# Performance work log

Measured on AMD Instinct MI355X. Metric: run time of the kernel, lower is better.

Reference implementation:

```python
import jax, jax.numpy as jnp
import numpy as np

N, Tq, Tk = 4096, 48, 48
E, H = 64, 4
HD = E // H
TN = 288            # time_num (5-min slots per day)
FE = 4              # forward_expansion
EPS = 1e-5


def _ln(x, g, b):
    mu = jnp.mean(x, axis=-1, keepdims=True)
    var = jnp.var(x, axis=-1, keepdims=True)
    return (x - mu) * jax.lax.rsqrt(var + EPS) * g + b


def setup_inputs() -> dict:
    rng = jax.random.key(0)
    ks = jax.random.split(rng, 12)
    s = 0.05
    return {
        "value": jax.random.normal(ks[0], (N, Tk, E), jnp.float32),
        "keys": jax.random.normal(ks[1], (N, Tk, E), jnp.float32),
        "query": jax.random.normal(ks[2], (N, Tq, E), jnp.float32),
        "Wv": jax.random.normal(ks[3], (HD, HD), jnp.float32) * s,
        "Wk": jax.random.normal(ks[4], (HD, HD), jnp.float32) * s,
        "Wq": jax.random.normal(ks[5], (HD, HD), jnp.float32) * s,
        "Wo": jax.random.normal(ks[6], (E, E), jnp.float32) * s,
        "bo": jnp.zeros((E,), jnp.float32),
        "temb": jax.random.normal(ks[7], (TN, E), jnp.float32) * s,
        "ln1_g": jnp.ones((E,), jnp.float32),
        "ln1_b": jnp.zeros((E,), jnp.float32),
        "ln2_g": jnp.ones((E,), jnp.float32),
        "ln2_b": jnp.zeros((E,), jnp.float32),
        "W1": jax.random.normal(ks[8], (FE * E, E), jnp.float32) * s,  # torch Linear(E, FE*E).weight
        "b1": jnp.zeros((FE * E,), jnp.float32),
        "W2": jax.random.normal(ks[9], (E, FE * E), jnp.float32) * s,
        "b2": jnp.zeros((E,), jnp.float32),
        "tq": 10,
    }


def reference(value, keys, query, Wv, Wk, Wq, Wo, bo, temb,
              ln1_g, ln1_b, ln2_g, ln2_b, W1, b1, W2, b2, tq):
    # temporal embedding add (tk = tq since tk=-1 default)
    tq_inds = (TN + tq + jnp.arange(Tq)) % TN
    tk_inds = (TN + tq + jnp.arange(Tk)) % TN
    q = query + temb[tq_inds][None, :, :]   # (N,Tq,E)
    k = keys + temb[tk_inds][None, :, :]    # (N,Tk,E)

    qh = q.reshape(N, Tq, H, HD)
    kh = k.reshape(N, Tk, H, HD)
    vh = value.reshape(N, Tk, H, HD)
    # per-head small linear projections (x @ W.T, no bias)
    qh = jnp.einsum('nthd,ed->nthe', qh, Wq)
    kh = jnp.einsum('nthd,ed->nthe', kh, Wk)
    vh = jnp.einsum('nthd,ed->nthe', vh, Wv)

    energy = jnp.einsum('nqhd,nkhd->nqkh', qh, kh)  # (N,Tq,Tk,H)
    # causal mask (mask=True path): masked entries set to -1e6 BEFORE scale+clamp
    tmask = jnp.tril(jnp.ones((Tq, Tk), jnp.float32))
    energy = jnp.where(tmask[None, :, :, None] == 0, jnp.float32(-1e6), energy)
    logits = jnp.clip(energy / jnp.float32(np.sqrt(E)), -5.0, 5.0)
    attention = jax.nn.softmax(logits, axis=2)       # softmax over k

    out = jnp.einsum('nqkh,nkhd->nqhd', attention, vh).reshape(N, Tq, E)
    out = out @ Wo.T + bo

    x = _ln(out + q, ln1_g, ln1_b)                   # dropout is identity (eval)
    ff = jax.nn.relu(x @ W1.T + b1) @ W2.T + b2
    return _ln(ff + x, ln2_g, ln2_b)
```

## Files before the change

kernel.cpp:

```cpp
#include <hip/hip_runtime.h>
#include <hip/hip_bf16.h>
#include <math.h>

#define NSEQ 4096
#define TN 288
#define EPSF 1e-5f

typedef short bf16x8 __attribute__((ext_vector_type(8)));
typedef float f32x4 __attribute__((ext_vector_type(4)));

#define WSV 0
#define WSK 256
#define WSQ 512
#define WSO 768
#define WS1 4864
#define WS2 21248

#define A_S   0
#define B_S   3456
#define C_S   6912
#define D_S   10496
#define CD_F  3456
#define H_S   6912

__device__ __forceinline__ unsigned short f2bf_u(float f) {
    __hip_bfloat16 h = __float2bfloat16(f);
    return *reinterpret_cast<const unsigned short*>(&h);
}
__device__ __forceinline__ unsigned int pk2(float a, float b) {
    return (unsigned int)f2bf_u(a) | ((unsigned int)f2bf_u(b) << 16);
}
__device__ __forceinline__ float bits2f(unsigned int u) { return __uint_as_float(u); }

__global__ void wconv_kernel(const float* __restrict__ Wv, const float* __restrict__ Wk,
                             const float* __restrict__ Wq, const float* __restrict__ Wo,
                             const float* __restrict__ W1, const float* __restrict__ W2,
                             short* __restrict__ ws) {
    int i = blockIdx.x * 256 + threadIdx.x;
    float v;
    if (i < 256)        v = Wv[i];
    else if (i < 512)   v = Wk[i - 256];
    else if (i < 768)   v = Wq[i - 512] * 0.125f;
    else if (i < 4864)  v = Wo[i - 768];
    else if (i < 21248) v = W1[i - 4864];
    else                v = W2[i - 21248];
    ws[i] = (short)f2bf_u(v);
}

__global__ __launch_bounds__(256, 5)
void ttrans_kernel(const float* __restrict__ value,
                   const float* __restrict__ keys,
                   const float* __restrict__ query,
                   const float* __restrict__ bo,
                   const float* __restrict__ temb,
                   const float* __restrict__ ln1g,
                   const float* __restrict__ ln1b,
                   const float* __restrict__ ln2g,
                   const float* __restrict__ ln2b,
                   const float* __restrict__ pb1,
                   const float* __restrict__ pb2,
                   const short* __restrict__ ws,
                   const int* __restrict__ tqp,
                   float* __restrict__ out)
{
    __shared__ __align__(16) unsigned char smem[27136];
    short* S16 = reinterpret_cast<short*>(smem);
    float* S32 = reinterpret_cast<float*>(smem);

    const int tid  = threadIdx.x;
    const int lane = tid & 63;
    const int w    = tid >> 6;
    const int l15  = lane & 15;
    const int lg   = lane >> 4;
    const int n    = blockIdx.x;
    const size_t gbase = (size_t)n * 3072;
    const int tqv  = *tqp;
    const int c4   = (lane & 15) * 4;
    const int rg   = lane >> 4;
    const int hh   = w;

    float4 qres4[3];
    {
        int t = w * 12 + rg;
        int ti = ((tqv % TN) + TN + t) % TN;
        #pragma unroll
        for (int it = 0; it < 3; ++it) {
            float4 tv = *reinterpret_cast<const float4*>(&temb[ti * 64 + c4]);
            float4 qv = *reinterpret_cast<const float4*>(&query[gbase + t * 64 + c4]);
            float4 kv = *reinterpret_cast<const float4*>(&keys [gbase + t * 64 + c4]);
            float4 vv = *reinterpret_cast<const float4*>(&value[gbase + t * 64 + c4]);
            float4 qq = make_float4(qv.x + tv.x, qv.y + tv.y, qv.z + tv.z, qv.w + tv.w);
            float4 kk = make_float4(kv.x + tv.x, kv.y + tv.y, kv.z + tv.z, kv.w + tv.w);
            qres4[it] = qq;
            *reinterpret_cast<uint2*>(&S16[A_S + t * 72 + c4]) =
                make_uint2(pk2(qq.x, qq.y), pk2(qq.z, qq.w));
            *reinterpret_cast<uint2*>(&S16[B_S + t * 72 + c4]) =
                make_uint2(pk2(kk.x, kk.y), pk2(kk.z, kk.w));
            *reinterpret_cast<uint2*>(&S16[C_S + t * 72 + c4]) =
                make_uint2(pk2(vv.x, vv.y), pk2(vv.z, vv.w));
            t += 4; ti += 4; if (ti >= TN) ti -= TN;
        }
    }
    __syncthreads();

    {
        bf16x8 bWv = {}, bWk = {}, bWq = {};
        if (lane < 32) {
            bWv = *reinterpret_cast<const bf16x8*>(&ws[WSV + l15 * 16 + lg * 8]);
            bWk = *reinterpret_cast<const bf16x8*>(&ws[WSK + l15 * 16 + lg * 8]);
            bWq = *reinterpret_cast<const bf16x8*>(&ws[WSQ + l15 * 16 + lg * 8]);
        }
        #pragma unroll
        for (int rt = 0; rt < 3; ++rt) {
            bf16x8 aQ = {}, aK = {}, aV = {};
            if (lane < 32) {
                int ro = (rt * 16 + l15) * 72 + hh * 16 + lg * 8;
                aQ = *reinterpret_cast<const bf16x8*>(&S16[A_S + ro]);
                aK = *reinterpret_cast<const bf16x8*>(&S16[B_S + ro]);
                aV = *reinterpret_cast<const bf16x8*>(&S16[C_S + ro]);
            }
            f32x4 z = {0.f,0.f,0.f,0.f};
            f32x4 cQ = __builtin_amdgcn_mfma_f32_16x16x32_bf16(aQ, bWq, z, 0, 0, 0);
            f32x4 cK = __builtin_amdgcn_mfma_f32_16x16x32_bf16(aK, bWk, z, 0, 0, 0);
            f32x4 cV = __builtin_amdgcn_mfma_f32_16x16x32_bf16(aV, bWv, z, 0, 0, 0);
            #pragma unroll
            for (int r = 0; r < 4; ++r) {
                int row = rt * 16 + lg * 4 + r;
                S16[A_S + row * 72 + hh * 16 + l15] = (short)f2bf_u(cQ[r]);
                S16[B_S + row * 72 + hh * 16 + l15] = (short)f2bf_u(cK[r]);
                S16[D_S + (hh * 16 + l15) * 48 + row] = (short)f2bf_u(cV[r]);
            }
        }
    }
    __syncthreads();

    {
        const float PEXP = 0.006737946999085467f;
        const unsigned short PBF = f2bf_u(PEXP);
        bf16x8 bK0 = {}, bK1 = {}, bK2 = {};
        if (lane < 32) {
            bK0 = *reinterpret_cast<const bf16x8*>(&S16[B_S + ( 0 + l15) * 72 + hh * 16 + lg * 8]);
            bK1 = *reinterpret_cast<const bf16x8*>(&S16[B_S + (16 + l15) * 72 + hh * 16 + lg * 8]);
            bK2 = *reinterpret_cast<const bf16x8*>(&S16[B_S + (32 + l15) * 72 + hh * 16 + lg * 8]);
        }
        bf16x8 vA = *reinterpret_cast<const bf16x8*>(&S16[D_S + (hh * 16 + l15) * 48 + lg * 8]);
        bf16x8 vB = {};
        if (lane < 32)
            vB = *reinterpret_cast<const bf16x8*>(&S16[D_S + (hh * 16 + l15) * 48 + 32 + lg * 8]);

        #pragma unroll
        for (int rt = 0; rt < 3; ++rt) {
            bf16x8 aQ = {};
            if (lane < 32)
                aQ = *reinterpret_cast<const bf16x8*>(&S16[A_S + (rt * 16 + l15) * 72 + hh * 16 + lg * 8]);
            f32x4 z = {0.f,0.f,0.f,0.f};
            f32x4 e0 = __builtin_amdgcn_mfma_f32_16x16x32_bf16(aQ, bK0, z, 0, 0, 0);
            f32x4 e1 = z, e2 = z;
            if (rt >= 1) e1 = __builtin_amdgcn_mfma_f32_16x16x32_bf16(aQ, bK1, z, 0, 0, 0);
            if (rt == 2) e2 = __builtin_amdgcn_mfma_f32_16x16x32_bf16(aQ, bK2, z, 0, 0, 0);
            const int abase = C_S + hh * 896;
            float inv[4];
            #pragma unroll
            for (int r = 0; r < 4; ++r) {
                int tl = lg * 4 + r;
                int t = rt * 16 + tl;
                float p0, p1, p2;
                float v0 = fminf(5.f, fmaxf(-5.f, e0[r]));
                if (rt == 0) v0 = (l15 <= t) ? v0 : -5.f;
                p0 = __expf(v0);
                S16[abase + tl * 56 + l15] = (short)f2bf_u(p0);
                if (rt == 0) {
                    p1 = PEXP;
                    S16[abase + tl * 56 + 16 + l15] = (short)PBF;
                } else {
                    float v1 = fminf(5.f, fmaxf(-5.f, e1[r]));
                    if (rt == 1) v1 = (16 + l15 <= t) ? v1 : -5.f;
                    p1 = __expf(v1);
                    S16[abase + tl * 56 + 16 + l15] = (short)f2bf_u(p1);
                }
                if (rt < 2) {
                    p2 = PEXP;
                    S16[abase + tl * 56 + 32 + l15] = (short)PBF;
                } else {
                    float v2c = fminf(5.f, fmaxf(-5.f, e2[r]));
                    v2c = (32 + l15 <= t) ? v2c : -5.f;
                    p2 = __expf(v2c);
                    S16[abase + tl * 56 + 32 + l15] = (short)f2bf_u(p2);
                }
                float s = p0 + p1 + p2;
                s += __shfl_xor(s, 1);
                s += __shfl_xor(s, 2);
                s += __shfl_xor(s, 4);
                s += __shfl_xor(s, 8);
                inv[r] = __builtin_amdgcn_rcpf(s);
            }
            bf16x8 a0 = *reinterpret_cast<const bf16x8*>(&S16[abase + l15 * 56 + lg * 8]);
            bf16x8 a1 = {};
            if (lane < 32)
                a1 = *reinterpret_cast<const bf16x8*>(&S16[abase + l15 * 56 + 32 + lg * 8]);
            f32x4 zz = {0.f,0.f,0.f,0.f};
            f32x4 oc = __builtin_amdgcn_mfma_f32_16x16x32_bf16(a0, vA, zz, 0, 0, 0);
            oc = __builtin_amdgcn_mfma_f32_16x16x32_bf16(a1, vB, oc, 0, 0, 0);
            #pragma unroll
            for (int r = 0; r < 4; ++r)
                S16[B_S + (rt * 16 + lg * 4 + r) * 72 + hh * 16 + l15] =
                    (short)f2bf_u(oc[r] * inv[r]);
        }
    }
    __syncthreads();

    {
        bf16x8 bO0 = *reinterpret_cast<const bf16x8*>(&ws[WSO + (w * 16 + l15) * 64 + lg * 8]);
        bf16x8 bO1 = *reinterpret_cast<const bf16x8*>(&ws[WSO + (w * 16 + l15) * 64 + 32 + lg * 8]);
        const float bo_v = bo[w * 16 + l15];
        #pragma unroll
        for (int mt = 0; mt < 3; ++mt) {
            bf16x8 a0 = *reinterpret_cast<const bf16x8*>(&S16[B_S + (mt * 16 + l15) * 72 + lg * 8]);
            bf16x8 a1 = *reinterpret_cast<const bf16x8*>(&S16[B_S + (mt * 16 + l15) * 72 + 32 + lg * 8]);
            f32x4 c = {0.f,0.f,0.f,0.f};
            c = __builtin_amdgcn_mfma_f32_16x16x32_bf16(a0, bO0, c, 0, 0, 0);
            c = __builtin_amdgcn_mfma_f32_16x16x32_bf16(a1, bO1, c, 0, 0, 0);
            #pragma unroll
            for (int r = 0; r < 4; ++r)
                S32[CD_F + (mt * 16 + lg * 4 + r) * 68 + w * 16 + l15] = c[r] + bo_v;
        }
    }
    __syncthreads();

    {
        float4 g1 = *reinterpret_cast<const float4*>(&ln1g[c4]);
        float4 be1 = *reinterpret_cast<const float4*>(&ln1b[c4]);
        #pragma unroll
        for (int it = 0; it < 3; ++it) {
            int t = w * 12 + it * 4 + rg;
            float4 o = *reinterpret_cast<const float4*>(&S32[CD_F + t * 68 + c4]);
            float v0 = o.x + qres4[it].x, v1 = o.y + qres4[it].y;
            float v2 = o.z + qres4[it].z, v3 = o.w + qres4[it].w;
            float s1 = (v0 + v1) + (v2 + v3);
            float s2 = (v0 * v0 + v1 * v1) + (v2 * v2 + v3 * v3);
            s1 += __shfl_xor(s1, 1); s1 += __shfl_xor(s1, 2);
            s1 += __shfl_xor(s1, 4); s1 += __shfl_xor(s1, 8);
            s2 += __shfl_xor(s2, 1); s2 += __shfl_xor(s2, 2);
            s2 += __shfl_xor(s2, 4); s2 += __shfl_xor(s2, 8);
            float mu  = s1 * (1.f / 64.f);
            float var = s2 * (1.f / 64.f) - mu * mu;
            float rs = __builtin_amdgcn_rsqf(var + EPSF);
            float x0 = (v0 - mu) * rs * g1.x + be1.x;
            float x1 = (v1 - mu) * rs * g1.y + be1.y;
            float x2 = (v2 - mu) * rs * g1.z + be1.z;
            float x3 = (v3 - mu) * rs * g1.w + be1.w;
            *reinterpret_cast<uint2*>(&S16[A_S + t * 72 + c4]) =
                make_uint2(pk2(x0, x1), pk2(x2, x3));
        }
    }
    __syncthreads();

    f32x4 ffC[3];
    #pragma unroll
    for (int mt = 0; mt < 3; ++mt) ffC[mt] = (f32x4){0.f,0.f,0.f,0.f};

    #pragma unroll
    for (int hb = 0; hb < 2; ++hb) {
        #pragma unroll
        for (int jj = 0; jj < 2; ++jj) {
            int j16 = w * 2 + jj;
            int jrow = (hb * 8 + j16) * 16 + l15;
            bf16x8 b0 = *reinterpret_cast<const bf16x8*>(&ws[WS1 + jrow * 64 + lg * 8]);
            bf16x8 b1 = *reinterpret_cast<const bf16x8*>(&ws[WS1 + jrow * 64 + 32 + lg * 8]);
            float b1v = pb1[jrow];
            #pragma unroll
            for (int mt = 0; mt < 3; ++mt) {
                bf16x8 a0 = *reinterpret_cast<const bf16x8*>(&S16[A_S + (mt * 16 + l15) * 72 + lg * 8]);
                bf16x8 a1 = *reinterpret_cast<const bf16x8*>(&S16[A_S + (mt * 16 + l15) * 72 + 32 + lg * 8]);
                f32x4 c = {0.f,0.f,0.f,0.f};
                c = __builtin_amdgcn_mfma_f32_16x16x32_bf16(a0, b0, c, 0, 0, 0);
                c = __builtin_amdgcn_mfma_f32_16x16x32_bf16(a1, b1, c, 0, 0, 0);
                #pragma unroll
                for (int r = 0; r < 4; ++r)
                    S16[H_S + (mt * 16 + lg * 4 + r) * 136 + j16 * 16 + l15] =
                        (short)f2bf_u(fmaxf(c[r] + b1v, 0.f));
            }
        }
        __syncthreads();

        {
            const int wb = WS2 + (w * 16 + l15) * 256 + hb * 128;
            bf16x8 bw0 = *reinterpret_cast<const bf16x8*>(&ws[wb +  0 + lg * 8]);
            bf16x8 bw1 = *reinterpret_cast<const bf16x8*>(&ws[wb + 32 + lg * 8]);
            bf16x8 bw2 = *reinterpret_cast<const bf16x8*>(&ws[wb + 64 + lg * 8]);
            bf16x8 bw3 = *reinterpret_cast<const bf16x8*>(&ws[wb + 96 + lg * 8]);
            #pragma unroll
            for (int mt = 0; mt < 3; ++mt) {
                bf16x8 a0 = *reinterpret_cast<const bf16x8*>(&S16[H_S + (mt * 16 + l15) * 136 +  0 + lg * 8]);
                bf16x8 a1 = *reinterpret_cast<const bf16x8*>(&S16[H_S + (mt * 16 + l15) * 136 + 32 + lg * 8]);
                bf16x8 a2 = *reinterpret_cast<const bf16x8*>(&S16[H_S + (mt * 16 + l15) * 136 + 64 + lg * 8]);
                bf16x8 a3 = *reinterpret_cast<const bf16x8*>(&S16[H_S + (mt * 16 + l15) * 136 + 96 + lg * 8]);
                ffC[mt] = __builtin_amdgcn_mfma_f32_16x16x32_bf16(a0, bw0, ffC[mt], 0, 0, 0);
                ffC[mt] = __builtin_amdgcn_mfma_f32_16x16x32_bf16(a1, bw1, ffC[mt], 0, 0, 0);
                ffC[mt] = __builtin_amdgcn_mfma_f32_16x16x32_bf16(a2, bw2, ffC[mt], 0, 0, 0);
                ffC[mt] = __builtin_amdgcn_mfma_f32_16x16x32_bf16(a3, bw3, ffC[mt], 0, 0, 0);
            }
        }
        if (hb == 0) __syncthreads();
    }

    {
        float b2v = pb2[w * 16 + l15];
        #pragma unroll
        for (int mt = 0; mt < 3; ++mt)
            #pragma unroll
            for (int r = 0; r < 4; ++r)
                S16[B_S + (mt * 16 + lg * 4 + r) * 72 + w * 16 + l15] =
                    (short)f2bf_u(ffC[mt][r] + b2v);
    }
    __syncthreads();

    {
        float4 g2 = *reinterpret_cast<const float4*>(&ln2g[c4]);
        float4 be2 = *reinterpret_cast<const float4*>(&ln2b[c4]);
        #pragma unroll
        for (int it = 0; it < 3; ++it) {
            int t = w * 12 + it * 4 + rg;
            uint2 fp = *reinterpret_cast<const uint2*>(&S16[B_S + t * 72 + c4]);
            uint2 xp = *reinterpret_cast<const uint2*>(&S16[A_S + t * 72 + c4]);
            float v0 = bits2f(fp.x << 16) + bits2f(xp.x << 16);
            float v1 = bits2f(fp.x & 0xffff0000u) + bits2f(xp.x & 0xffff0000u);
            float v2 = bits2f(fp.y << 16) + bits2f(xp.y << 16);
            float v3 = bits2f(fp.y & 0xffff0000u) + bits2f(xp.y & 0xffff0000u);
            float s1 = (v0 + v1) + (v2 + v3);
            float s2 = (v0 * v0 + v1 * v1) + (v2 * v2 + v3 * v3);
            s1 += __shfl_xor(s1, 1); s1 += __shfl_xor(s1, 2);
            s1 += __shfl_xor(s1, 4); s1 += __shfl_xor(s1, 8);
            s2 += __shfl_xor(s2, 1); s2 += __shfl_xor(s2, 2);
            s2 += __shfl_xor(s2, 4); s2 += __shfl_xor(s2, 8);
            float mu  = s1 * (1.f / 64.f);
            float var = s2 * (1.f / 64.f) - mu * mu;
            float rs = __builtin_amdgcn_rsqf(var + EPSF);
            float y0 = (v0 - mu) * rs * g2.x + be2.x;
            float y1 = (v1 - mu) * rs * g2.y + be2.y;
            float y2 = (v2 - mu) * rs * g2.z + be2.z;
            float y3 = (v3 - mu) * rs * g2.w + be2.w;
            *reinterpret_cast<float4*>(&out[gbase + t * 64 + c4]) =
                make_float4(y0, y1, y2, y3);
        }
    }
}

extern "C" void kernel_launch(void* const* d_in, const int* in_sizes, int n_in,
                              void* d_out, int out_size, void* d_ws, size_t ws_size,
                              hipStream_t stream) {
    const float* value = (const float*)d_in[0];
    const float* keys  = (const float*)d_in[1];
    const float* query = (const float*)d_in[2];
    const float* Wv    = (const float*)d_in[3];
    const float* Wk    = (const float*)d_in[4];
    const float* Wq    = (const float*)d_in[5];
    const float* Wo    = (const float*)d_in[6];
    const float* bo    = (const float*)d_in[7];
    const float* temb  = (const float*)d_in[8];
    const float* ln1g  = (const float*)d_in[9];
    const float* ln1b  = (const float*)d_in[10];
    const float* ln2g  = (const float*)d_in[11];
    const float* ln2b  = (const float*)d_in[12];
    const float* W1    = (const float*)d_in[13];
    const float* b1    = (const float*)d_in[14];
    const float* W2    = (const float*)d_in[15];
    const float* b2    = (const float*)d_in[16];
    const int*   tq    = (const int*)d_in[17];
    float* outp = (float*)d_out;
    short* ws = (short*)d_ws;

    hipLaunchKernelGGL(wconv_kernel, dim3(147), dim3(256), 0, stream,
                       Wv, Wk, Wq, Wo, W1, W2, ws);
    hipLaunchKernelGGL(ttrans_kernel, dim3(NSEQ), dim3(256), 0, stream,
                       value, keys, query, bo, temb,
                       ln1g, ln1b, ln2g, ln2b, b1, b2, ws, tq, outp);
}
```

Baseline: 74.99 us.

## Make each warp own a row tile through Wo, LN1, FFN and LN2

After attention, the output projection, first layernorm, both FFN matmuls and the final layernorm are restructured so each of three waves owns a 16-row tile and covers all 64 output columns. This drops the block-wide barriers between these stages and the fp32 smem staging buffer, and keeps the LN1 output in registers for the second residual. The Q projection result is also kept in registers and written to a compact per-head smem area so the A buffer can hold the raw q residual. The cost is that the fourth wave sits idle for the whole tail, each wave does four times the FFN MFMA work serially, and the final stores become scalar strided writes instead of float4.

```diff
diff --git a/kernel.cpp b/kernel.cpp
--- a/kernel.cpp
+++ b/kernel.cpp
@@ -20,7 +20,6 @@
 #define B_S   3456
 #define C_S   6912
 #define D_S   10496
-#define CD_F  3456
 #define H_S   6912
 
 __device__ __forceinline__ unsigned short f2bf_u(float f) {
@@ -65,7 +64,6 @@
 {
     __shared__ __align__(16) unsigned char smem[27136];
     short* S16 = reinterpret_cast<short*>(smem);
-    float* S32 = reinterpret_cast<float*>(smem);
 
     const int tid  = threadIdx.x;
     const int lane = tid & 63;
@@ -79,7 +77,6 @@
     const int rg   = lane >> 4;
     const int hh   = w;
 
-    float4 qres4[3];
     {
         int t = w * 12 + rg;
         int ti = ((tqv % TN) + TN + t) % TN;
@@ -91,7 +88,6 @@
             float4 vv = *reinterpret_cast<const float4*>(&value[gbase + t * 64 + c4]);
             float4 qq = make_float4(qv.x + tv.x, qv.y + tv.y, qv.z + tv.z, qv.w + tv.w);
             float4 kk = make_float4(kv.x + tv.x, kv.y + tv.y, kv.z + tv.z, kv.w + tv.w);
-            qres4[it] = qq;
             *reinterpret_cast<uint2*>(&S16[A_S + t * 72 + c4]) =
                 make_uint2(pk2(qq.x, qq.y), pk2(qq.z, qq.w));
             *reinterpret_cast<uint2*>(&S16[B_S + t * 72 + c4]) =
@@ -103,6 +99,7 @@
     }
     __syncthreads();
 
+    f32x4 cQ[3];
     {
         bf16x8 bWv = {}, bWk = {}, bWq = {};
         if (lane < 32) {
@@ -120,13 +117,12 @@
                 aV = *reinterpret_cast<const bf16x8*>(&S16[C_S + ro]);
             }
             f32x4 z = {0.f,0.f,0.f,0.f};
-            f32x4 cQ = __builtin_amdgcn_mfma_f32_16x16x32_bf16(aQ, bWq, z, 0, 0, 0);
+            cQ[rt] = __builtin_amdgcn_mfma_f32_16x16x32_bf16(aQ, bWq, z, 0, 0, 0);
             f32x4 cK = __builtin_amdgcn_mfma_f32_16x16x32_bf16(aK, bWk, z, 0, 0, 0);
             f32x4 cV = __builtin_amdgcn_mfma_f32_16x16x32_bf16(aV, bWv, z, 0, 0, 0);
             #pragma unroll
             for (int r = 0; r < 4; ++r) {
                 int row = rt * 16 + lg * 4 + r;
-                S16[A_S + row * 72 + hh * 16 + l15] = (short)f2bf_u(cQ[r]);
                 S16[B_S + row * 72 + hh * 16 + l15] = (short)f2bf_u(cK[r]);
                 S16[D_S + (hh * 16 + l15) * 48 + row] = (short)f2bf_u(cV[r]);
             }
@@ -137,6 +133,12 @@
     {
         const float PEXP = 0.006737946999085467f;
         const unsigned short PBF = f2bf_u(PEXP);
+        #pragma unroll
+        for (int rt = 0; rt < 3; ++rt)
+            #pragma unroll
+            for (int r = 0; r < 4; ++r)
+                S16[C_S + hh * 768 + (rt * 16 + lg * 4 + r) * 16 + l15] =
+                    (short)f2bf_u(cQ[rt][r]);
         bf16x8 bK0 = {}, bK1 = {}, bK2 = {};
         if (lane < 32) {
             bK0 = *reinterpret_cast<const bf16x8*>(&S16[B_S + ( 0 + l15) * 72 + hh * 16 + lg * 8]);
@@ -152,13 +154,13 @@
         for (int rt = 0; rt < 3; ++rt) {
             bf16x8 aQ = {};
             if (lane < 32)
-                aQ = *reinterpret_cast<const bf16x8*>(&S16[A_S + (rt * 16 + l15) * 72 + hh * 16 + lg * 8]);
+                aQ = *reinterpret_cast<const bf16x8*>(&S16[C_S + hh * 768 + (rt * 16 + l15) * 16 + lg * 8]);
             f32x4 z = {0.f,0.f,0.f,0.f};
             f32x4 e0 = __builtin_amdgcn_mfma_f32_16x16x32_bf16(aQ, bK0, z, 0, 0, 0);
             f32x4 e1 = z, e2 = z;
             if (rt >= 1) e1 = __builtin_amdgcn_mfma_f32_16x16x32_bf16(aQ, bK1, z, 0, 0, 0);
             if (rt == 2) e2 = __builtin_amdgcn_mfma_f32_16x16x32_bf16(aQ, bK2, z, 0, 0, 0);
-            const int abase = C_S + hh * 896;
+            const int abase = D_S + hh * 768;
             float inv[4];
             #pragma unroll
             for (int r = 0; r < 4; ++r) {
@@ -168,24 +170,24 @@
                 float v0 = fminf(5.f, fmaxf(-5.f, e0[r]));
                 if (rt == 0) v0 = (l15 <= t) ? v0 : -5.f;
                 p0 = __expf(v0);
-                S16[abase + tl * 56 + l15] = (short)f2bf_u(p0);
+                S16[abase + tl * 48 + l15] = (short)f2bf_u(p0);
                 if (rt == 0) {
                     p1 = PEXP;
-                    S16[abase + tl * 56 + 16 + l15] = (short)PBF;
+                    S16[abase + tl * 48 + 16 + l15] = (short)PBF;
                 } else {
                     float v1 = fminf(5.f, fmaxf(-5.f, e1[r]));
                     if (rt == 1) v1 = (16 + l15 <= t) ? v1 : -5.f;
                     p1 = __expf(v1);
-                    S16[abase + tl * 56 + 16 + l15] = (short)f2bf_u(p1);
+                    S16[abase + tl * 48 + 16 + l15] = (short)f2bf_u(p1);
                 }
                 if (rt < 2) {
                     p2 = PEXP;
-                    S16[abase + tl * 56 + 32 + l15] = (short)PBF;
+                    S16[abase + tl * 48 + 32 + l15] = (short)PBF;
                 } else {
                     float v2c = fminf(5.f, fmaxf(-5.f, e2[r]));
                     v2c = (32 + l15 <= t) ? v2c : -5.f;
                     p2 = __expf(v2c);
-                    S16[abase + tl * 56 + 32 + l15] = (short)f2bf_u(p2);
+                    S16[abase + tl * 48 + 32 + l15] = (short)f2bf_u(p2);
                 }
                 float s = p0 + p1 + p2;
                 s += __shfl_xor(s, 1);
@@ -194,10 +196,10 @@
                 s += __shfl_xor(s, 8);
                 inv[r] = __builtin_amdgcn_rcpf(s);
             }
-            bf16x8 a0 = *reinterpret_cast<const bf16x8*>(&S16[abase + l15 * 56 + lg * 8]);
+            bf16x8 a0 = *reinterpret_cast<const bf16x8*>(&S16[abase + l15 * 48 + lg * 8]);
             bf16x8 a1 = {};
             if (lane < 32)
-                a1 = *reinterpret_cast<const bf16x8*>(&S16[abase + l15 * 56 + 32 + lg * 8]);
+                a1 = *reinterpret_cast<const bf16x8*>(&S16[abase + l15 * 48 + 32 + lg * 8]);
             f32x4 zz = {0.f,0.f,0.f,0.f};
             f32x4 oc = __builtin_amdgcn_mfma_f32_16x16x32_bf16(a0, vA, zz, 0, 0, 0);
             oc = __builtin_amdgcn_mfma_f32_16x16x32_bf16(a1, vB, oc, 0, 0, 0);
@@ -209,35 +211,37 @@
     }
     __syncthreads();
 
-    {
-        bf16x8 bO0 = *reinterpret_cast<const bf16x8*>(&ws[WSO + (w * 16 + l15) * 64 + lg * 8]);
-        bf16x8 bO1 = *reinterpret_cast<const bf16x8*>(&ws[WSO + (w * 16 + l15) * 64 + 32 + lg * 8]);
-        const float bo_v = bo[w * 16 + l15];
-        #pragma unroll
-        for (int mt = 0; mt < 3; ++mt) {
-            bf16x8 a0 = *reinterpret_cast<const bf16x8*>(&S16[B_S + (mt * 16 + l15) * 72 + lg * 8]);
-            bf16x8 a1 = *reinterpret_cast<const bf16x8*>(&S16[B_S + (mt * 16 + l15) * 72 + 32 + lg * 8]);
-            f32x4 c = {0.f,0.f,0.f,0.f};
-            c = __builtin_amdgcn_mfma_f32_16x16x32_bf16(a0, bO0, c, 0, 0, 0);
-            c = __builtin_amdgcn_mfma_f32_16x16x32_bf16(a1, bO1, c, 0, 0, 0);
-            #pragma unroll
-            for (int r = 0; r < 4; ++r)
-                S32[CD_F + (mt * 16 + lg * 4 + r) * 68 + w * 16 + l15] = c[r] + bo_v;
-        }
-    }
-    __syncthreads();
-
-    {
-        float4 g1 = *reinterpret_cast<const float4*>(&ln1g[c4]);
-        float4 be1 = *reinterpret_cast<const float4*>(&ln1b[c4]);
-        #pragma unroll
-        for (int it = 0; it < 3; ++it) {
-            int t = w * 12 + it * 4 + rg;
-            float4 o = *reinterpret_cast<const float4*>(&S32[CD_F + t * 68 + c4]);
-            float v0 = o.x + qres4[it].x, v1 = o.y + qres4[it].y;
-            float v2 = o.z + qres4[it].z, v3 = o.w + qres4[it].w;
-            float s1 = (v0 + v1) + (v2 + v3);
-            float s2 = (v0 * v0 + v1 * v1) + (v2 * v2 + v3 * v3);
+    if (w < 3) {
+        bf16x8 ao0 = *reinterpret_cast<const bf16x8*>(&S16[B_S + (w * 16 + l15) * 72 + lg * 8]);
+        bf16x8 ao1 = *reinterpret_cast<const bf16x8*>(&S16[B_S + (w * 16 + l15) * 72 + 32 + lg * 8]);
+        f32x4 c[4];
+        #pragma unroll
+        for (int nt = 0; nt < 4; ++nt) {
+            bf16x8 bO0 = *reinterpret_cast<const bf16x8*>(&ws[WSO + (nt * 16 + l15) * 64 + lg * 8]);
+            bf16x8 bO1 = *reinterpret_cast<const bf16x8*>(&ws[WSO + (nt * 16 + l15) * 64 + 32 + lg * 8]);
+            f32x4 z = {0.f,0.f,0.f,0.f};
+            c[nt] = __builtin_amdgcn_mfma_f32_16x16x32_bf16(ao0, bO0, z, 0, 0, 0);
+            c[nt] = __builtin_amdgcn_mfma_f32_16x16x32_bf16(ao1, bO1, c[nt], 0, 0, 0);
+        }
+        float bo4[4], g1v[4], be1v[4];
+        #pragma unroll
+        for (int nt = 0; nt < 4; ++nt) {
+            bo4[nt]  = bo[nt * 16 + l15];
+            g1v[nt]  = ln1g[nt * 16 + l15];
+            be1v[nt] = ln1b[nt * 16 + l15];
+        }
+        float xres[4][4];
+        #pragma unroll
+        for (int r = 0; r < 4; ++r) {
+            int row = w * 16 + lg * 4 + r;
+            float v[4];
+            #pragma unroll
+            for (int nt = 0; nt < 4; ++nt) {
+                unsigned int qb = (unsigned int)(unsigned short)S16[A_S + row * 72 + nt * 16 + l15];
+                v[nt] = c[nt][r] + bo4[nt] + bits2f(qb << 16);
+            }
+            float s1 = (v[0] + v[1]) + (v[2] + v[3]);
+            float s2 = (v[0]*v[0] + v[1]*v[1]) + (v[2]*v[2] + v[3]*v[3]);
             s1 += __shfl_xor(s1, 1); s1 += __shfl_xor(s1, 2);
             s1 += __shfl_xor(s1, 4); s1 += __shfl_xor(s1, 8);
             s2 += __shfl_xor(s2, 1); s2 += __shfl_xor(s2, 2);
@@ -245,90 +249,67 @@
             float mu  = s1 * (1.f / 64.f);
             float var = s2 * (1.f / 64.f) - mu * mu;
             float rs = __builtin_amdgcn_rsqf(var + EPSF);
-            float x0 = (v0 - mu) * rs * g1.x + be1.x;
-            float x1 = (v1 - mu) * rs * g1.y + be1.y;
-            float x2 = (v2 - mu) * rs * g1.z + be1.z;
-            float x3 = (v3 - mu) * rs * g1.w + be1.w;
-            *reinterpret_cast<uint2*>(&S16[A_S + t * 72 + c4]) =
-                make_uint2(pk2(x0, x1), pk2(x2, x3));
-        }
-    }
-    __syncthreads();
-
-    f32x4 ffC[3];
-    #pragma unroll
-    for (int mt = 0; mt < 3; ++mt) ffC[mt] = (f32x4){0.f,0.f,0.f,0.f};
-
-    #pragma unroll
-    for (int hb = 0; hb < 2; ++hb) {
-        #pragma unroll
-        for (int jj = 0; jj < 2; ++jj) {
-            int j16 = w * 2 + jj;
-            int jrow = (hb * 8 + j16) * 16 + l15;
-            bf16x8 b0 = *reinterpret_cast<const bf16x8*>(&ws[WS1 + jrow * 64 + lg * 8]);
-            bf16x8 b1 = *reinterpret_cast<const bf16x8*>(&ws[WS1 + jrow * 64 + 32 + lg * 8]);
-            float b1v = pb1[jrow];
-            #pragma unroll
-            for (int mt = 0; mt < 3; ++mt) {
-                bf16x8 a0 = *reinterpret_cast<const bf16x8*>(&S16[A_S + (mt * 16 + l15) * 72 + lg * 8]);
-                bf16x8 a1 = *reinterpret_cast<const bf16x8*>(&S16[A_S + (mt * 16 + l15) * 72 + 32 + lg * 8]);
-                f32x4 c = {0.f,0.f,0.f,0.f};
-                c = __builtin_amdgcn_mfma_f32_16x16x32_bf16(a0, b0, c, 0, 0, 0);
-                c = __builtin_amdgcn_mfma_f32_16x16x32_bf16(a1, b1, c, 0, 0, 0);
+            #pragma unroll
+            for (int nt = 0; nt < 4; ++nt) {
+                float x = (v[nt] - mu) * rs * g1v[nt] + be1v[nt];
+                xres[r][nt] = x;
+                S16[A_S + row * 72 + nt * 16 + l15] = (short)f2bf_u(x);
+            }
+        }
+        f32x4 ffC[4];
+        #pragma unroll
+        for (int nt = 0; nt < 4; ++nt) ffC[nt] = (f32x4){0.f,0.f,0.f,0.f};
+        bf16x8 aX0 = *reinterpret_cast<const bf16x8*>(&S16[A_S + (w * 16 + l15) * 72 + lg * 8]);
+        bf16x8 aX1 = *reinterpret_cast<const bf16x8*>(&S16[A_S + (w * 16 + l15) * 72 + 32 + lg * 8]);
+        #pragma unroll
+        for (int hb = 0; hb < 2; ++hb) {
+            #pragma unroll
+            for (int j16 = 0; j16 < 8; ++j16) {
+                int jrow = (hb * 8 + j16) * 16 + l15;
+                bf16x8 b0 = *reinterpret_cast<const bf16x8*>(&ws[WS1 + jrow * 64 + lg * 8]);
+                bf16x8 b1 = *reinterpret_cast<const bf16x8*>(&ws[WS1 + jrow * 64 + 32 + lg * 8]);
+                float b1v = pb1[jrow];
+                f32x4 z = {0.f,0.f,0.f,0.f};
+                f32x4 ch = __builtin_amdgcn_mfma_f32_16x16x32_bf16(aX0, b0, z, 0, 0, 0);
+                ch = __builtin_amdgcn_mfma_f32_16x16x32_bf16(aX1, b1, ch, 0, 0, 0);
                 #pragma unroll
                 for (int r = 0; r < 4; ++r)
-                    S16[H_S + (mt * 16 + lg * 4 + r) * 136 + j16 * 16 + l15] =
-                        (short)f2bf_u(fmaxf(c[r] + b1v, 0.f));
-            }
-        }
-        __syncthreads();
-
-        {
-            const int wb = WS2 + (w * 16 + l15) * 256 + hb * 128;
-            bf16x8 bw0 = *reinterpret_cast<const bf16x8*>(&ws[wb +  0 + lg * 8]);
-            bf16x8 bw1 = *reinterpret_cast<const bf16x8*>(&ws[wb + 32 + lg * 8]);
-            bf16x8 bw2 = *reinterpret_cast<const bf16x8*>(&ws[wb + 64 + lg * 8]);
-            bf16x8 bw3 = *reinterpret_cast<const bf16x8*>(&ws[wb + 96 + lg * 8]);
-            #pragma unroll
-            for (int mt = 0; mt < 3; ++mt) {
-                bf16x8 a0 = *reinterpret_cast<const bf16x8*>(&S16[H_S + (mt * 16 + l15) * 136 +  0 + lg * 8]);
-                bf16x8 a1 = *reinterpret_cast<const bf16x8*>(&S16[H_S + (mt * 16 + l15) * 136 + 32 + lg * 8]);
-                bf16x8 a2 = *reinterpret_cast<const bf16x8*>(&S16[H_S + (mt * 16 + l15) * 136 + 64 + lg * 8]);
-                bf16x8 a3 = *reinterpret_cast<const bf16x8*>(&S16[H_S + (mt * 16 + l15) * 136 + 96 + lg * 8]);
-                ffC[mt] = __builtin_amdgcn_mfma_f32_16x16x32_bf16(a0, bw0, ffC[mt], 0, 0, 0);
-                ffC[mt] = __builtin_amdgcn_mfma_f32_16x16x32_bf16(a1, bw1, ffC[mt], 0, 0, 0);
-                ffC[mt] = __builtin_amdgcn_mfma_f32_16x16x32_bf16(a2, bw2, ffC[mt], 0, 0, 0);
-                ffC[mt] = __builtin_amdgcn_mfma_f32_16x16x32_bf16(a3, bw3, ffC[mt], 0, 0, 0);
-            }
-        }
-        if (hb == 0) __syncthreads();
-    }
-
-    {
-        float b2v = pb2[w * 16 + l15];
-        #pragma unroll
-        for (int mt = 0; mt < 3; ++mt)
-            #pragma unroll
-            for (int r = 0; r < 4; ++r)
-                S16[B_S + (mt * 16 + lg * 4 + r) * 72 + w * 16 + l15] =
-                    (short)f2bf_u(ffC[mt][r] + b2v);
-    }
-    __syncthreads();
-
-    {
-        float4 g2 = *reinterpret_cast<const float4*>(&ln2g[c4]);
-        float4 be2 = *reinterpret_cast<const float4*>(&ln2b[c4]);
-        #pragma unroll
-        for (int it = 0; it < 3; ++it) {
-            int t = w * 12 + it * 4 + rg;
-            uint2 fp = *reinterpret_cast<const uint2*>(&S16[B_S + t * 72 + c4]);
-            uint2 xp = *reinterpret_cast<const uint2*>(&S16[A_S + t * 72 + c4]);
-            float v0 = bits2f(fp.x << 16) + bits2f(xp.x << 16);
-            float v1 = bits2f(fp.x & 0xffff0000u) + bits2f(xp.x & 0xffff0000u);
-            float v2 = bits2f(fp.y << 16) + bits2f(xp.y << 16);
-            float v3 = bits2f(fp.y & 0xffff0000u) + bits2f(xp.y & 0xffff0000u);
-            float s1 = (v0 + v1) + (v2 + v3);
-            float s2 = (v0 * v0 + v1 * v1) + (v2 * v2 + v3 * v3);
+                    S16[H_S + (w * 16 + lg * 4 + r) * 136 + j16 * 16 + l15] =
+                        (short)f2bf_u(fmaxf(ch[r] + b1v, 0.f));
+            }
+            bf16x8 aH0 = *reinterpret_cast<const bf16x8*>(&S16[H_S + (w * 16 + l15) * 136 +  0 + lg * 8]);
+            bf16x8 aH1 = *reinterpret_cast<const bf16x8*>(&S16[H_S + (w * 16 + l15) * 136 + 32 + lg * 8]);
+            bf16x8 aH2 = *reinterpret_cast<const bf16x8*>(&S16[H_S + (w * 16 + l15) * 136 + 64 + lg * 8]);
+            bf16x8 aH3 = *reinterpret_cast<const bf16x8*>(&S16[H_S + (w * 16 + l15) * 136 + 96 + lg * 8]);
+            #pragma unroll
+            for (int nt = 0; nt < 4; ++nt) {
+                const int wb = WS2 + (nt * 16 + l15) * 256 + hb * 128;
+                bf16x8 bw0 = *reinterpret_cast<const bf16x8*>(&ws[wb +  0 + lg * 8]);
+                bf16x8 bw1 = *reinterpret_cast<const bf16x8*>(&ws[wb + 32 + lg * 8]);
+                bf16x8 bw2 = *reinterpret_cast<const bf16x8*>(&ws[wb + 64 + lg * 8]);
+                bf16x8 bw3 = *reinterpret_cast<const bf16x8*>(&ws[wb + 96 + lg * 8]);
+                ffC[nt] = __builtin_amdgcn_mfma_f32_16x16x32_bf16(aH0, bw0, ffC[nt], 0, 0, 0);
+                ffC[nt] = __builtin_amdgcn_mfma_f32_16x16x32_bf16(aH1, bw1, ffC[nt], 0, 0, 0);
+                ffC[nt] = __builtin_amdgcn_mfma_f32_16x16x32_bf16(aH2, bw2, ffC[nt], 0, 0, 0);
+                ffC[nt] = __builtin_amdgcn_mfma_f32_16x16x32_bf16(aH3, bw3, ffC[nt], 0, 0, 0);
+            }
+        }
+        float b2v4[4], g2v[4], be2v[4];
+        #pragma unroll
+        for (int nt = 0; nt < 4; ++nt) {
+            b2v4[nt] = pb2[nt * 16 + l15];
+            g2v[nt]  = ln2g[nt * 16 + l15];
+            be2v[nt] = ln2b[nt * 16 + l15];
+        }
+        #pragma unroll
+        for (int r = 0; r < 4; ++r) {
+            int row = w * 16 + lg * 4 + r;
+            float v[4];
+            #pragma unroll
+            for (int nt = 0; nt < 4; ++nt)
+                v[nt] = ffC[nt][r] + b2v4[nt] + xres[r][nt];
+            float s1 = (v[0] + v[1]) + (v[2] + v[3]);
+            float s2 = (v[0]*v[0] + v[1]*v[1]) + (v[2]*v[2] + v[3]*v[3]);
             s1 += __shfl_xor(s1, 1); s1 += __shfl_xor(s1, 2);
             s1 += __shfl_xor(s1, 4); s1 += __shfl_xor(s1, 8);
             s2 += __shfl_xor(s2, 1); s2 += __shfl_xor(s2, 2);
@@ -336,12 +317,10 @@
             float mu  = s1 * (1.f / 64.f);
             float var = s2 * (1.f / 64.f) - mu * mu;
             float rs = __builtin_amdgcn_rsqf(var + EPSF);
-            float y0 = (v0 - mu) * rs * g2.x + be2.x;
-            float y1 = (v1 - mu) * rs * g2.y + be2.y;
-            float y2 = (v2 - mu) * rs * g2.z + be2.z;
-            float y3 = (v3 - mu) * rs * g2.w + be2.w;
-            *reinterpret_cast<float4*>(&out[gbase + t * 64 + c4]) =
-                make_float4(y0, y1, y2, y3);
+            #pragma unroll
+            for (int nt = 0; nt < 4; ++nt)
+                out[gbase + row * 64 + nt * 16 + l15] =
+                    (v[nt] - mu) * rs * g2v[nt] + be2v[nt];
         }
     }
 }
```

After: 131.2 us. 1.75x slower.
